# Performance work log

Hardware: AMD Instinct MI355X
Metric: run time of the kernel (lower is better)

## Reference

```python
import jax, jax.numpy as jnp
import numpy as np

N = 256          # spatial_dim
NC = 3           # components: u, v, density
INNER = 10       # inner_steps
DX = 2.0 * np.pi / N
VISC = 1e-3


def _van_leer(r):
    # classic van Leer limiter: (r+|r|)/(1+|r|)
    return jnp.where(r > 0, 2.0 * r / (1.0 + r), 0.0)


def _advect(c, u, v, dt):
    """van-Leer flux-limited advection tendency -div(vel*c) on a periodic grid.
    TVD blend of upwind (low-order) and Lax-Wendroff (high-order) face fluxes."""
    tend = jnp.zeros_like(c)
    for ax, vel in ((-2, u), (-1, v)):
        uf = 0.5 * (vel + jnp.roll(vel, -1, ax))   # face velocity at i+1/2
        cn = jnp.roll(c, -1, ax)
        dc = cn - c
        f_low = jnp.where(uf >= 0, uf * c, uf * cn)                      # upwind
        f_high = uf * 0.5 * (c + cn) - 0.5 * uf * uf * (dt / DX) * dc    # Lax-Wendroff
        dc_up = jnp.where(uf >= 0, c - jnp.roll(c, 1, ax), jnp.roll(c, -2, ax) - cn)
        dc_safe = jnp.where(jnp.abs(dc) > 1e-12, dc, 1e-12)
        phi = _van_leer(dc_up / dc_safe)
        flux = f_low + phi * (f_high - f_low)
        tend = tend - (flux - jnp.roll(flux, 1, ax)) / DX
    return tend


def _laplacian(x):
    return (jnp.roll(x, 1, -1) + jnp.roll(x, -1, -1)
            + jnp.roll(x, 1, -2) + jnp.roll(x, -1, -2) - 4.0 * x) / (DX * DX)


def _inv_fd_laplacian_eigs():
    # eigenvalues of the periodic FD laplacian, pseudo-inverse (zero mean mode)
    k = np.arange(N)
    lam1 = (2.0 * np.cos(2.0 * np.pi * k / N) - 2.0) / (DX * DX)
    lam = lam1[:, None] + lam1[None, :]
    lam[0, 0] = 1.0
    inv = 1.0 / lam
    inv[0, 0] = 0.0
    return jnp.asarray(inv, dtype=jnp.float32)

_INV_LAM = _inv_fd_laplacian_eigs()


def _project(u, v):
    """Pressure projection: remove divergence via FFT Poisson solve (periodic)."""
    div = (u - jnp.roll(u, 1, -2)) / DX + (v - jnp.roll(v, 1, -1)) / DX  # backward diff
    q = jnp.real(jnp.fft.ifft2(jnp.fft.fft2(div) * _INV_LAM))
    gu = (jnp.roll(q, -1, -2) - q) / DX   # forward diff (adjoint of div)
    gv = (jnp.roll(q, -1, -1) - q) / DX
    return u - gu, v - gv


def _inner_step(state, dt):
    u, v, d = state
    # velocity: explicit van-Leer convection + explicit diffusion, then projection
    u1 = u + dt * (_advect(u, u, v, dt) + VISC * _laplacian(u))
    v1 = v + dt * (_advect(v, u, v, dt) + VISC * _laplacian(v))
    u1, v1 = _project(u1, v1)
    # density advected with the OLD velocity (matches module's inner_step_fn)
    d1 = d + dt * _advect(d, u, v, dt)
    return (u1, v1, d1)


def _repeated_step(state, dt):
    def body(s, _):
        return _inner_step(s, dt), None
    state, _ = jax.lax.scan(body, state, None, length=INNER)
    return state


def setup_inputs() -> dict:
    key = jax.random.key(0)
    y0 = 0.1 * jax.random.normal(key, (8, N * N * NC), dtype=jnp.float32)
    return {"y0": y0, "dt": jnp.float32(1e-3), "num_steps_forward": 8}


def reference(y0, dt, num_steps_forward):
    spatial = y0.reshape(-1, N, N, NC)           # [B,H,W,3]
    state0 = (spatial[..., 0], spatial[..., 1], spatial[..., 2])

    def body(s, _):
        s2 = _repeated_step(s, dt)
        return s2, s2
    _, traj = jax.lax.scan(body, state0, None, length=num_steps_forward)
    yt = jnp.stack(traj, axis=-1)                # [T,B,H,W,3]
    yt = jnp.swapaxes(yt, 0, 1)                  # [B,T,H,W,3]
    return yt.reshape(yt.shape[0], yt.shape[1], N * N * NC)
```

## Files before the change

### kernel.cpp

```cpp
#include <hip/hip_runtime.h>
#include <hip/hip_bf16.h>


#define NN 256
#define NM 255
#define FIELD (NN*NN)
#define BATCH 8
#define TOTAL (BATCH*FIELD)
#define ROWF2 264

constexpr float RDX  = 40.743665431525205f;
constexpr float VISC = 1e-3f;

__device__ __forceinline__ int rev8(int x) { return (int)(__brev((unsigned)x) >> 24); }
__device__ __forceinline__ int pdx(int x)  { return x + (x >> 5); }

__device__ __forceinline__ void wave_sync() {
  asm volatile("" ::: "memory");
  __builtin_amdgcn_wave_barrier();
}

__device__ __forceinline__ float decode_dt(const unsigned* dtw) {
  unsigned w = dtw[0];
  float cf = __uint_as_float(w);
  float cb = __uint_as_float((w & 0xFFFFu) << 16);
  bool v32 = (cf > 1e-8f) && (cf < 1.0f);
  bool vbf = (cb > 1e-8f) && (cb < 1.0f);
  return v32 ? cf : (vbf ? cb : 1e-3f);
}

__device__ __forceinline__ float face_flux(float uf, float cm, float c0,
                                           float cp, float cpp, float hdtdx) {
  float dc = cp - c0;
  float f_low  = (uf >= 0.0f) ? uf*c0 : uf*cp;
  float f_high = uf*0.5f*(c0+cp) - hdtdx*uf*uf*dc;
  float dc_up  = (uf >= 0.0f) ? (c0 - cm) : (cpp - cp);
  float dc_safe = (fabsf(dc) > 1e-12f) ? dc : 1e-12f;
  float phi = (dc_up * dc_safe > 0.0f) ? (2.0f*dc_up/(dc_up + dc_safe)) : 0.0f;
  return f_low + phi*(f_high - f_low);
}

template<int NEED_VD>
__device__ __forceinline__ void advect_point(
    const float* __restrict__ Ub, const float* __restrict__ Vb,
    const float* __restrict__ Db,
    int i, int j, float hdtdx, float dt,
    float& u1, float& v1, float& d1)
{
  int im2 = ((i-2)&NM)*NN, im1 = ((i-1)&NM)*NN, i0r = i*NN,
      ip1 = ((i+1)&NM)*NN, ip2 = ((i+2)&NM)*NN;
  int jm2 = (j-2)&NM, jm1 = (j-1)&NM, jp1 = (j+1)&NM, jp2 = (j+2)&NM;

  float u_c  = Ub[i0r+j];
  float u_im2= Ub[im2+j], u_im1 = Ub[im1+j], u_ip1 = Ub[ip1+j], u_ip2 = Ub[ip2+j];
  float u_jm2= Ub[i0r+jm2], u_jm1 = Ub[i0r+jm1], u_jp1 = Ub[i0r+jp1], u_jp2 = Ub[i0r+jp2];
  float v_c  = Vb[i0r+j];
  float v_jm1= Vb[i0r+jm1], v_jp1 = Vb[i0r+jp1];

  float ufI0 = 0.5f*(u_c + u_ip1);
  float ufIm = 0.5f*(u_im1 + u_c);
  float vfJ0 = 0.5f*(v_c + v_jp1);
  float vfJm = 0.5f*(v_jm1 + v_c);

  float tu = -(( face_flux(ufI0, u_im1, u_c, u_ip1, u_ip2, hdtdx)
               - face_flux(ufIm, u_im2, u_im1, u_c, u_ip1, hdtdx))
             + ( face_flux(vfJ0, u_jm1, u_c, u_jp1, u_jp2, hdtdx)
               - face_flux(vfJm, u_jm2, u_jm1, u_c, u_jp1, hdtdx))) * RDX;
  float lapu = (u_im1 + u_ip1 + u_jm1 + u_jp1 - 4.0f*u_c) * (RDX*RDX);
  u1 = u_c + dt*(tu + VISC*lapu);

  if (NEED_VD) {
    float v_im2= Vb[im2+j], v_im1 = Vb[im1+j], v_ip1 = Vb[ip1+j], v_ip2 = Vb[ip2+j];
    float v_jm2= Vb[i0r+jm2], v_jp2 = Vb[i0r+jp2];
    float d_c  = Db[i0r+j];
    float d_im2= Db[im2+j], d_im1 = Db[im1+j], d_ip1 = Db[ip1+j], d_ip2 = Db[ip2+j];
    float d_jm2= Db[i0r+jm2], d_jm1 = Db[i0r+jm1], d_jp1 = Db[i0r+jp1], d_jp2 = Db[i0r+jp2];

    float tv = -(( face_flux(ufI0, v_im1, v_c, v_ip1, v_ip2, hdtdx)
                 - face_flux(ufIm, v_im2, v_im1, v_c, v_ip1, hdtdx))
               + ( face_flux(vfJ0, v_jm1, v_c, v_jp1, v_jp2, hdtdx)
                 - face_flux(vfJm, v_jm2, v_jm1, v_c, v_jp1, hdtdx))) * RDX;
    float lapv = (v_im1 + v_ip1 + v_jm1 + v_jp1 - 4.0f*v_c) * (RDX*RDX);
    v1 = v_c + dt*(tv + VISC*lapv);

    float td = -(( face_flux(ufI0, d_im1, d_c, d_ip1, d_ip2, hdtdx)
                 - face_flux(ufIm, d_im2, d_im1, d_c, d_ip1, hdtdx))
               + ( face_flux(vfJ0, d_jm1, d_c, d_jp1, d_jp2, hdtdx)
                 - face_flux(vfJm, d_jm2, d_jm1, d_c, d_jp1, hdtdx))) * RDX;
    d1 = d_c + dt*td;
  }
}

template<int NEED_VD>
__device__ __forceinline__ void advect_point_lds(
    const float* __restrict__ U, const float* __restrict__ V,
    const float* __restrict__ D,
    int ku, int kv, int j, float hdtdx, float dt,
    float& u1, float& v1, float& d1)
{
  int jm2 = (j-2)&NM, jm1 = (j-1)&NM, jp1 = (j+1)&NM, jp2 = (j+2)&NM;

  const float* Ur = U + ku*NN;
  float u_c  = Ur[j];
  float u_im2= U[(ku-2)*NN+j], u_im1 = U[(ku-1)*NN+j],
        u_ip1= U[(ku+1)*NN+j], u_ip2 = U[(ku+2)*NN+j];
  float u_jm2= Ur[jm2], u_jm1 = Ur[jm1], u_jp1 = Ur[jp1], u_jp2 = Ur[jp2];
  const float* Vr = V + kv*NN;
  float v_c  = Vr[j];
  float v_jm1= Vr[jm1], v_jp1 = Vr[jp1];

  float ufI0 = 0.5f*(u_c + u_ip1);
  float ufIm = 0.5f*(u_im1 + u_c);
  float vfJ0 = 0.5f*(v_c + v_jp1);
  float vfJm = 0.5f*(v_jm1 + v_c);

  float tu = -(( face_flux(ufI0, u_im1, u_c, u_ip1, u_ip2, hdtdx)
               - face_flux(ufIm, u_im2, u_im1, u_c, u_ip1, hdtdx))
             + ( face_flux(vfJ0, u_jm1, u_c, u_jp1, u_jp2, hdtdx)
               - face_flux(vfJm, u_jm2, u_jm1, u_c, u_jp1, hdtdx))) * RDX;
  float lapu = (u_im1 + u_ip1 + u_jm1 + u_jp1 - 4.0f*u_c) * (RDX*RDX);
  u1 = u_c + dt*(tu + VISC*lapu);

  if (NEED_VD) {
    float v_im2= V[(kv-2)*NN+j], v_im1 = V[(kv-1)*NN+j],
          v_ip1= V[(kv+1)*NN+j], v_ip2 = V[(kv+2)*NN+j];
    float v_jm2= Vr[jm2], v_jp2 = Vr[jp2];
    const float* Dr = D + kv*NN;
    float d_c  = Dr[j];
    float d_im2= D[(kv-2)*NN+j], d_im1 = D[(kv-1)*NN+j],
          d_ip1= D[(kv+1)*NN+j], d_ip2 = D[(kv+2)*NN+j];
    float d_jm2= Dr[jm2], d_jm1 = Dr[jm1], d_jp1 = Dr[jp1], d_jp2 = Dr[jp2];

    float tv = -(( face_flux(ufI0, v_im1, v_c, v_ip1, v_ip2, hdtdx)
                 - face_flux(ufIm, v_im2, v_im1, v_c, v_ip1, hdtdx))
               + ( face_flux(vfJ0, v_jm1, v_c, v_jp1, v_jp2, hdtdx)
                 - face_flux(vfJm, v_jm2, v_jm1, v_c, v_jp1, hdtdx))) * RDX;
    float lapv = (v_im1 + v_ip1 + v_jm1 + v_jp1 - 4.0f*v_c) * (RDX*RDX);
    v1 = v_c + dt*(tv + VISC*lapv);

    float td = -(( face_flux(ufI0, d_im1, d_c, d_ip1, d_ip2, hdtdx)
                 - face_flux(ufIm, d_im2, d_im1, d_c, d_ip1, hdtdx))
               + ( face_flux(vfJ0, d_jm1, d_c, d_jp1, d_jp2, hdtdx)
                 - face_flux(vfJm, d_jm2, d_jm1, d_c, d_jp1, hdtdx))) * RDX;
    d1 = d_c + dt*td;
  }
}


__device__ __forceinline__ void r16_fwd_low(float2* x, const float2* tw) {
  #pragma unroll
  for (int s = 1; s <= 4; ++s) {
    int h = 1 << (s-1);
    #pragma unroll
    for (int b = 0; b < 8; ++b) {
      int q = b & (h-1);
      int t = ((b >> (s-1)) << s) + q;
      float2 w = tw[q << (8-s)];
      float2 a = x[t], c = x[t+h];
      float wbx = w.x*c.x - w.y*c.y, wby = w.x*c.y + w.y*c.x;
      x[t]   = make_float2(a.x+wbx, a.y+wby);
      x[t+h] = make_float2(a.x-wbx, a.y-wby);
    }
  }
}
__device__ __forceinline__ void r16_fwd_high(float2* x, int r, const float2* tw) {
  #pragma unroll
  for (int s = 5; s <= 8; ++s) {
    int hp = 1 << (s-5);
    #pragma unroll
    for (int b = 0; b < 8; ++b) {
      int qp = b & (hp-1);
      int t = ((b >> (s-5)) << (s-4)) + qp;
      float2 w = tw[(r + (qp<<4)) << (8-s)];
      float2 a = x[t], c = x[t+hp];
      float wbx = w.x*c.x - w.y*c.y, wby = w.x*c.y + w.y*c.x;
      x[t]    = make_float2(a.x+wbx, a.y+wby);
      x[t+hp] = make_float2(a.x-wbx, a.y-wby);
    }
  }
}
__device__ __forceinline__ void r16_inv_high(float2* x, int r, const float2* tw) {
  #pragma unroll
  for (int s = 8; s >= 5; --s) {
    int hp = 1 << (s-5);
    #pragma unroll
    for (int b = 0; b < 8; ++b) {
      int qp = b & (hp-1);
      int t = ((b >> (s-5)) << (s-4)) + qp;
      float2 w = tw[(r + (qp<<4)) << (8-s)];
      float2 a = x[t], c = x[t+hp];
      float dx = a.x-c.x, dy = a.y-c.y;
      x[t]    = make_float2(a.x+c.x, a.y+c.y);
      x[t+hp] = make_float2(w.x*dx + w.y*dy, w.x*dy - w.y*dx);
    }
  }
}
__device__ __forceinline__ void r16_inv_low(float2* x, const float2* tw) {
  #pragma unroll
  for (int s = 4; s >= 1; --s) {
    int h = 1 << (s-1);
    #pragma unroll
    for (int b = 0; b < 8; ++b) {
      int q = b & (h-1);
      int t = ((b >> (s-1)) << s) + q;
      float2 w = tw[q << (8-s)];
      float2 a = x[t], c = x[t+h];
      float dx = a.x-c.x, dy = a.y-c.y;
      x[t]   = make_float2(a.x+c.x, a.y+c.y);
      x[t+h] = make_float2(w.x*dx + w.y*dy, w.x*dy - w.y*dx);
    }
  }
}

__device__ __forceinline__ void fft256_fwd_f2(float2* __restrict__ A, int lane,
                                              const float2* __restrict__ tw,
                                              bool active)
{
  #pragma unroll
  for (int s = 1; s <= 8; s += 2) {
    if (active) {
      int half = 1 << (s-1);
      int q2 = lane & (half - 1);
      int i0 = ((lane >> (s-1)) << (s+1)) + q2;
      float2 a0 = A[pdx(i0)];
      float2 a1 = A[pdx(i0 + half)];
      float2 a2 = A[pdx(i0 + 2*half)];
      float2 a3 = A[pdx(i0 + 3*half)];
      float2 w1 = tw[q2 << (8 - s)];
      float wbx = w1.x*a1.x - w1.y*a1.y, wby = w1.x*a1.y + w1.y*a1.x;
      float2 b0 = make_float2(a0.x + wbx, a0.y + wby);
      float2 b1 = make_float2(a0.x - wbx, a0.y - wby);
      wbx = w1.x*a3.x - w1.y*a3.y; wby = w1.x*a3.y + w1.y*a3.x;
      float2 b2 = make_float2(a2.x + wbx, a2.y + wby);
      float2 b3 = make_float2(a2.x - wbx, a2.y - wby);
      float2 w2 = tw[q2 << (7 - s)];
      float2 w3 = tw[(q2 + half) << (7 - s)];
      wbx = w2.x*b2.x - w2.y*b2.y; wby = w2.x*b2.y + w2.y*b2.x;
      A[pdx(i0)]            = make_float2(b0.x + wbx, b0.y + wby);
      A[pdx(i0 + 2*half)]   = make_float2(b0.x - wbx, b0.y - wby);
      wbx = w3.x*b3.x - w3.y*b3.y; wby = w3.x*b3.y + w3.y*b3.x;
      A[pdx(i0 + half)]     = make_float2(b1.x + wbx, b1.y + wby);
      A[pdx(i0 + 3*half)]   = make_float2(b1.x - wbx, b1.y - wby);
    }
    wave_sync();
  }
}

__device__ __forceinline__ void fft256_inv_f2(float2* __restrict__ A, int lane,
                                              const float2* __restrict__ tw,
                                              bool active)
{
  #pragma unroll
  for (int s = 8; s >= 2; s -= 2) {
    if (active) {
      int h = 1 << (s-2);
      int q2 = lane & (h - 1);
      int i0 = ((lane >> (s-2)) << s) + q2;
      float2 a0 = A[pdx(i0)];
      float2 a1 = A[pdx(i0 + h)];
      float2 a2 = A[pdx(i0 + 2*h)];
      float2 a3 = A[pdx(i0 + 3*h)];
      float2 w1 = tw[q2 << (8 - s)];
      float2 w2 = tw[(q2 + h) << (8 - s)];
      float dx = a0.x - a2.x, dy = a0.y - a2.y;
      float2 b0 = make_float2(a0.x + a2.x, a0.y + a2.y);
      float2 b2 = make_float2(w1.x*dx + w1.y*dy, w1.x*dy - w1.y*dx);
      dx = a1.x - a3.x; dy = a1.y - a3.y;
      float2 b1 = make_float2(a1.x + a3.x, a1.y + a3.y);
      float2 b3 = make_float2(w2.x*dx + w2.y*dy, w2.x*dy - w2.y*dx);
      float2 w3 = tw[q2 << (9 - s)];
      dx = b0.x - b1.x; dy = b0.y - b1.y;
      A[pdx(i0)]       = make_float2(b0.x + b1.x, b0.y + b1.y);
      A[pdx(i0 + h)]   = make_float2(w3.x*dx + w3.y*dy, w3.x*dy - w3.y*dx);
      dx = b2.x - b3.x; dy = b2.y - b3.y;
      A[pdx(i0 + 2*h)] = make_float2(b2.x + b3.x, b2.y + b3.y);
      A[pdx(i0 + 3*h)] = make_float2(w3.x*dx + w3.y*dy, w3.x*dy - w3.y*dx);
    }
    wave_sync();
  }
}

template<int W>
__device__ __forceinline__ void fft256_dit_fwd(float2* __restrict__ A, int lane,
                                               const float2* __restrict__ tw,
                                               bool active)
{
  #pragma unroll
  for (int s = 1; s <= 8; ++s) {
    int half = 1 << (s-1);
    if (active) {
      #pragma unroll
      for (int r = 0; r < 128/W; ++r) {
        int bfly = lane + r*W;
        int q = bfly & (half - 1);
        int g = (bfly >> (s-1)) << s;
        float2 w = tw[q << (8 - s)];
        float2 a = A[pdx(g + q)];
        float2 b = A[pdx(g + q + half)];
        float wbx = w.x*b.x - w.y*b.y;
        float wby = w.x*b.y + w.y*b.x;
        A[pdx(g + q)]        = make_float2(a.x + wbx, a.y + wby);
        A[pdx(g + q + half)] = make_float2(a.x - wbx, a.y - wby);
      }
    }
    wave_sync();
  }
}

template<int W>
__device__ __forceinline__ void fft256_dif_inv(float2* __restrict__ A, int lane,
                                               const float2* __restrict__ tw,
                                               bool active)
{
  #pragma unroll
  for (int s = 8; s >= 1; --s) {
    int half = 1 << (s-1);
    if (active) {
      #pragma unroll
      for (int r = 0; r < 128/W; ++r) {
        int bfly = lane + r*W;
        int q = bfly & (half - 1);
        int g = (bfly >> (s-1)) << s;
        float2 w = tw[q << (8 - s)];
        float2 a = A[pdx(g + q)];
        float2 b = A[pdx(g + q + half)];
        float dx = a.x - b.x, dy = a.y - b.y;
        A[pdx(g + q)]        = make_float2(a.x + b.x, a.y + b.y);
        A[pdx(g + q + half)] = make_float2(w.x*dx + w.y*dy, w.x*dy - w.y*dx);
      }
    }
    wave_sync();
  }
}

__global__ __launch_bounds__(1024) void proj_advect_fft8(
    const float2* __restrict__ Sprev, const float* __restrict__ inb,
    float* __restrict__ outb, float2* __restrict__ Snew,
    float* __restrict__ out, const unsigned* __restrict__ dtw,
    int T, int tm1, int first)
{
  __shared__ float2 tw[128];
  __shared__ float2 AbS[14*ROWF2];
  __shared__ float  qs [14*NN];
  __shared__ float  Ucs[13*NN];
  __shared__ float  Vcs[12*NN];
  float* Dss = (float*)(AbS + 8*ROWF2);
  float* Vs  = qs;

  const int tid  = threadIdx.x;
  const int j    = tid & 255;
  const int qtr  = tid >> 8;
  const int b    = blockIdx.x >> 5;
  const int row0 = (blockIdx.x & 31) << 3;

  if (tid < 128) {
    float sw, cw;
    __sincosf(-0.02454369260617026f * (float)tid, &sw, &cw);
    tw[tid] = make_float2(cw, sw);
  }

  const float dt = decode_dt(dtw);
  const float hdtdx = 0.5f*dt*RDX;

  const float* Ub = inb + b*FIELD;
  const float* Vb = inb + TOTAL + b*FIELD;
  const float* Db = inb + 2*TOTAL + b*FIELD;
  float* Uo  = outb + b*FIELD;
  float* Vo  = outb + TOTAL + b*FIELD;
  float* Do_ = outb + 2*TOTAL + b*FIELD;

  float u_reg[4], v_reg[3], d_reg[3];
  #pragma unroll
  for (int m = 0; m < 4; ++m) {
    int e = tid + (m << 10);
    if (e < 13*NN) {
      int k = e >> 8, jj = e & 255;
      u_reg[m] = Ub[((row0 - 3 + k) & NM)*NN + jj];
    }
  }
  #pragma unroll
  for (int m = 0; m < 3; ++m) {
    int e = tid + (m << 10);
    int k = e >> 8, jj = e & 255;
    int gr = ((row0 - 2 + k) & NM)*NN;
    v_reg[m] = Vb[gr + jj];
    d_reg[m] = Db[gr + jj];
  }

  if (!first) {
    const float2* Sb = Sprev + b*FIELD;
    #pragma unroll
    for (int m = 0; m < 4; ++m) {
      int e = tid + (m << 10);
      if (e < 14*NN) {
        int k = e >> 8, jj = e & 255;
        AbS[k*ROWF2 + pdx(jj)] = Sb[((row0 - 3 + k) & NM)*NN + jj];
      }
    }
    __syncthreads();

    {
      const int g16 = tid >> 4;
      const int r   = tid & 15;
      if (g16 < 14) {
        float2* Ar = AbS + g16*ROWF2;
        float2 x[16];
        #pragma unroll
        for (int k = 0; k < 16; ++k) x[k] = Ar[pdx(r + (k<<4))];
        r16_inv_high(x, r, tw);
        #pragma unroll
        for (int k = 0; k < 16; ++k) Ar[pdx(r + (k<<4))] = x[k];
      }
      wave_sync();
      if (g16 < 14) {
        float2* Ar = AbS + g16*ROWF2;
        float2 x[16];
        #pragma unroll
        for (int t = 0; t < 16; ++t) x[t] = Ar[pdx((r<<4) + t)];
        r16_inv_low(x, tw);
        #pragma unroll
        for (int t = 0; t < 16; ++t) Ar[pdx((r<<4) + t)] = x[t];
      }
    }
    __syncthreads();

    #pragma unroll
    for (int m = 0; m < 4; ++m) {
      int e = tid + (m << 10);
      if (e < 14*NN) {
        int k = e >> 8, jj = e & 255;
        qs[k*NN + jj] = AbS[k*ROWF2 + pdx(rev8(jj))].x;
      }
    }
    __syncthreads();
  } else {
    __syncthreads();
  }

  #pragma unroll
  for (int m = 0; m < 4; ++m) {
    int e = tid + (m << 10);
    if (e < 13*NN) {
      int k = e >> 8, jj = e & 255;
      Ucs[e] = first ? u_reg[m]
                     : (u_reg[m] - (qs[(k+1)*NN + jj] - qs[k*NN + jj])*RDX);
    }
  }
  #pragma unroll
  for (int m = 0; m < 3; ++m) {
    int e = tid + (m << 10);
    int k = e >> 8, jj = e & 255;
    Vcs[e] = first ? v_reg[m]
                   : (v_reg[m] - (qs[(k+1)*NN + ((jj+1)&NM)] - qs[(k+1)*NN + jj])*RDX);
    Dss[e] = d_reg[m];
  }
  __syncthreads();

  if (tm1 >= 0) {
    #pragma unroll
    for (int m = 0; m < 2; ++m) {
      int e = tid + (m << 10);
      int k = e >> 8, jj = e & 255;
      int pos = (row0 + k)*NN + jj;
      size_t o = ((size_t)(b*T + tm1)*FIELD + pos)*3u;
      out[o]   = Ucs[(k+3)*NN + jj];
      out[o+1] = Vcs[(k+2)*NN + jj];
      out[o+2] = Dss[(k+2)*NN + jj];
    }
  }

  const int kbeg = (qtr << 1) - 1;
  float u1r[3];
  #pragma unroll
  for (int kk = 0; kk < 3; ++kk) {
    int k = kbeg + kk;
    int ku = k + 3, kv = k + 2;
    float u1, v1, d1;
    if (kk == 0) {
      advect_point_lds<0>(Ucs, Vcs, Dss, ku, kv, j, hdtdx, dt, u1, v1, d1);
    } else {
      advect_point_lds<1>(Ucs, Vcs, Dss, ku, kv, j, hdtdx, dt, u1, v1, d1);
      int gi = (row0 + k)*NN + j;
      Uo[gi] = u1; Vo[gi] = v1; Do_[gi] = d1;
      Vs[k*NN + j] = v1;
    }
    u1r[kk] = u1;
  }
  __syncthreads();

  {
    int jm1 = (j - 1) & NM, rj = rev8(j);
    #pragma unroll
    for (int m = 0; m < 2; ++m) {
      int k = (qtr << 1) + m;
      float dv = (u1r[m+1] - u1r[m] + Vs[k*NN + j] - Vs[k*NN + jm1]) * RDX;
      AbS[k*ROWF2 + pdx(rj)] = make_float2(dv, 0.0f);
    }
  }
  __syncthreads();

  {
    const int g16 = tid >> 4;
    const int r   = tid & 15;
    if (g16 < 8) {
      float2* Ar = AbS + g16*ROWF2;
      float2 x[16];
      #pragma unroll
      for (int t = 0; t < 16; ++t) x[t] = Ar[pdx((r<<4) + t)];
      r16_fwd_low(x, tw);
      #pragma unroll
      for (int t = 0; t < 16; ++t) Ar[pdx((r<<4) + t)] = x[t];
    }
    wave_sync();
    if (g16 < 8) {
      float2* Ar = AbS + g16*ROWF2;
      float2 x[16];
      #pragma unroll
      for (int k = 0; k < 16; ++k) x[k] = Ar[pdx(r + (k<<4))];
      r16_fwd_high(x, r, tw);
      #pragma unroll
      for (int k = 0; k < 16; ++k) Ar[pdx(r + (k<<4))] = x[k];
    }
  }
  __syncthreads();

  float2* So = Snew + b*FIELD;
  #pragma unroll
  for (int m = 0; m < 2; ++m) {
    int e = tid + (m << 10);
    int row = e >> 8, jj = e & 255;
    So[(row0 + row)*NN + jj] = AbS[row*ROWF2 + pdx(jj)];
  }
}

__global__ __launch_bounds__(512) void fft_cols(float2* __restrict__ S)
{
  __shared__ float2 Ab[8*ROWF2];
  __shared__ float2 tw[128];
  __shared__ float  lam[NN];
  int tid = threadIdx.x;
  int b = blockIdx.x >> 5;
  int col0 = (blockIdx.x & 31) << 3;

  if (tid < 128) {
    float sw, cw;
    __sincosf(-0.02454369260617026f * (float)tid, &sw, &cw);
    tw[tid] = make_float2(cw, sw);
  }
  if (tid < 256) {
    float s1 = __sinf(0.01227184630308512983f * (float)tid);
    lam[tid] = -4.0f * s1 * s1 * (RDX*RDX);
  }

  float2* Sb = S + b*FIELD;
  #pragma unroll
  for (int k = 0; k < 4; ++k) {
    int idx = tid + (k << 9);
    int i = idx >> 3, c = idx & 7;
    Ab[c*ROWF2 + pdx(rev8(i))] = Sb[i*NN + col0 + c];
  }
  __syncthreads();

  int g = tid >> 6, lane = tid & 63;
  fft256_fwd_f2(Ab + g*ROWF2, lane, tw, true);

  float l2 = lam[col0 + g];
  #pragma unroll
  for (int r = 0; r < 4; ++r) {
    int k1 = lane + (r << 6);
    float den = lam[k1] + l2;
    float sc = ((k1 | (col0 + g)) == 0) ? 0.0f : (1.0f/den);
    sc *= (1.0f/65536.0f);
    float2 v = Ab[g*ROWF2 + pdx(k1)];
    Ab[g*ROWF2 + pdx(k1)] = make_float2(v.x*sc, v.y*sc);
  }
  wave_sync();

  fft256_inv_f2(Ab + g*ROWF2, lane, tw, true);
  __syncthreads();

  #pragma unroll
  for (int k = 0; k < 4; ++k) {
    int idx = tid + (k << 9);
    int i = idx >> 3, c = idx & 7;
    Sb[i*NN + col0 + c] = Ab[c*ROWF2 + pdx(rev8(i))];
  }
}

__global__ __launch_bounds__(512) void advect_div_fft(
    const float* __restrict__ inb, float* __restrict__ outb,
    float2* __restrict__ S, float* __restrict__ out,
    const unsigned* __restrict__ dtw, int T, int tm1)
{
  __shared__ float  Vs[8][NN];
  __shared__ float2 AbS[8*ROWF2];
  __shared__ float2 tw[128];
  const int tid = threadIdx.x;
  const int j   = tid & 255;
  const int h   = tid >> 8;
  const int b    = blockIdx.x >> 5;
  const int row0 = (blockIdx.x & 31) << 3;

  if (tid < 128) {
    float sw, cw;
    __sincosf(-0.02454369260617026f * (float)tid, &sw, &cw);
    tw[tid] = make_float2(cw, sw);
  }

  const float* Ub = inb + b*FIELD;
  const float* Vb = inb + TOTAL + b*FIELD;
  const float* Db = inb + 2*TOTAL + b*FIELD;
  float* Uo  = outb + b*FIELD;
  float* Vo  = outb + TOTAL + b*FIELD;
  float* Do_ = outb + 2*TOTAL + b*FIELD;

  const float dt = decode_dt(dtw);
  const float hdtdx = 0.5f*dt*RDX;

  if (tm1 >= 0) {
    #pragma unroll
    for (int k = 0; k < 4; ++k) {
      int pos = (row0 + h*4 + k)*NN + j;
      size_t o = ((size_t)(b*T + tm1)*FIELD + pos)*3u;
      out[o]   = Ub[pos];
      out[o+1] = Vb[pos];
      out[o+2] = Db[pos];
    }
  }

  const int kbeg = h ? 3 : -1;
  float u1r[5];
  #pragma unroll
  for (int kk = 0; kk < 5; ++kk) {
    int k = kbeg + kk;
    int r = (row0 + k) & NM;
    float u1, v1, d1;
    if (kk == 0) {
      advect_point<0>(Ub, Vb, Db, r, j, hdtdx, dt, u1, v1, d1);
    } else {
      advect_point<1>(Ub, Vb, Db, r, j, hdtdx, dt, u1, v1, d1);
      int gi = r*NN + j;
      Uo[gi] = u1; Vo[gi] = v1; Do_[gi] = d1;
      Vs[k][j] = v1;
    }
    u1r[kk] = u1;
  }
  __syncthreads();

  {
    int jm1 = (j - 1) & NM, rj = rev8(j);
    #pragma unroll
    for (int m = 0; m < 4; ++m) {
      int k = h*4 + m;
      float dv = (u1r[m+1] - u1r[m] + Vs[k][j] - Vs[k][jm1]) * RDX;
      AbS[k*ROWF2 + pdx(rj)] = make_float2(dv, 0.0f);
    }
  }
  __syncthreads();

  const int g = tid >> 6, lane = tid & 63;
  fft256_dit_fwd<64>(AbS + g*ROWF2, lane, tw, true);
  __syncthreads();

  float2* Sb = S + b*FIELD;
  #pragma unroll
  for (int k = 0; k < 4; ++k) {
    int row = h*4 + k;
    Sb[(row0 + row)*NN + j] = AbS[row*ROWF2 + pdx(j)];
  }
}

__global__ __launch_bounds__(512) void fft_cols_r9(float2* __restrict__ S)
{
  __shared__ float2 Ab[8*ROWF2];
  __shared__ float2 tw[128];
  __shared__ float  lam[NN];
  int tid = threadIdx.x;
  int b = blockIdx.x >> 5;
  int col0 = (blockIdx.x & 31) << 3;

  if (tid < 128) {
    float sw, cw;
    __sincosf(-0.02454369260617026f * (float)tid, &sw, &cw);
    tw[tid] = make_float2(cw, sw);
  }
  if (tid < 256) {
    float s1 = __sinf(0.01227184630308512983f * (float)tid);
    lam[tid] = -4.0f * s1 * s1 * (RDX*RDX);
  }

  float2* Sb = S + b*FIELD;
  #pragma unroll
  for (int k = 0; k < 4; ++k) {
    int idx = tid + (k << 9);
    int i = idx >> 3, c = idx & 7;
    Ab[c*ROWF2 + pdx(rev8(i))] = Sb[i*NN + col0 + c];
  }
  __syncthreads();

  int g = tid >> 6, lane = tid & 63;
  fft256_dit_fwd<64>(Ab + g*ROWF2, lane, tw, true);

  float l2 = lam[col0 + g];
  #pragma unroll
  for (int r = 0; r < 4; ++r) {
    int k1 = lane + (r << 6);
    float den = lam[k1] + l2;
    float sc = ((k1 | (col0 + g)) == 0) ? 0.0f : (1.0f/den);
    sc *= (1.0f/65536.0f);
    float2 v = Ab[g*ROWF2 + pdx(k1)];
    Ab[g*ROWF2 + pdx(k1)] = make_float2(v.x*sc, v.y*sc);
  }
  wave_sync();

  fft256_dif_inv<64>(Ab + g*ROWF2, lane, tw, true);
  __syncthreads();

  #pragma unroll
  for (int k = 0; k < 4; ++k) {
    int idx = tid + (k << 9);
    int i = idx >> 3, c = idx & 7;
    Sb[i*NN + col0 + c] = Ab[c*ROWF2 + pdx(rev8(i))];
  }
}

__global__ __launch_bounds__(512) void fft_inv_correct(
    const float2* __restrict__ S, float* __restrict__ outb)
{
  __shared__ float2 Ab[9*ROWF2];
  __shared__ float  qs[9*NN];
  __shared__ float2 tw[128];
  int tid = threadIdx.x;
  int b = blockIdx.x >> 5;
  int row0 = (blockIdx.x & 31) << 3;

  if (tid < 128) {
    float sw, cw;
    __sincosf(-0.02454369260617026f * (float)tid, &sw, &cw);
    tw[tid] = make_float2(cw, sw);
  }

  const float2* Sb = S + b*FIELD;
  #pragma unroll
  for (int m = 0; m < 5; ++m) {
    int e = tid + m*512;
    if (e < 9*NN) {
      int k = e >> 8, j = e & 255;
      Ab[k*ROWF2 + pdx(j)] = Sb[((row0 + k) & NM)*NN + j];
    }
  }
  __syncthreads();

  int g = tid >> 5, lane = tid & 31;
  bool active = (g < 9);
  fft256_dif_inv<32>(Ab + (active ? g : 8)*ROWF2, lane, tw, active);
  __syncthreads();

  #pragma unroll
  for (int m = 0; m < 5; ++m) {
    int e = tid + m*512;
    if (e < 9*NN) {
      int k = e >> 8, j = e & 255;
      qs[k*NN + j] = Ab[k*ROWF2 + pdx(rev8(j))].x;
    }
  }
  __syncthreads();

  float* Ug = outb + b*FIELD;
  float* Vg = outb + TOTAL + b*FIELD;
  #pragma unroll
  for (int m = 0; m < 4; ++m) {
    int e = tid + m*512;
    int k = e >> 8, j = e & 255;
    int gi = (row0 + k)*NN + j;
    float q0 = qs[k*NN + j];
    float q1 = qs[(k+1)*NN + j];
    float qj = qs[k*NN + ((j+1) & NM)];
    Ug[gi] -= (q1 - q0)*RDX;
    Vg[gi] -= (qj - q0)*RDX;
  }
}

__global__ __launch_bounds__(256) void write_out_k(
    const float* __restrict__ U, const float* __restrict__ V, const float* __restrict__ D,
    float* __restrict__ out, int t, int T)
{
  int idx = blockIdx.x*256 + threadIdx.x;
  int b = idx >> 16;
  int pos = idx & (FIELD-1);
  size_t o = ((size_t)(b*T + t)*FIELD + pos)*3u;
  out[o]   = U[idx];
  out[o+1] = V[idx];
  out[o+2] = D[idx];
}

__global__ __launch_bounds__(256) void init_state(
    const float* __restrict__ y0,
    float* __restrict__ U, float* __restrict__ V, float* __restrict__ D)
{
  int idx = blockIdx.x*256 + threadIdx.x;
  U[idx] = y0[idx*3];
  V[idx] = y0[idx*3+1];
  D[idx] = y0[idx*3+2];
}

__device__ __forceinline__ void fft_fwd_sc(float2* A, int lane) {
  #pragma unroll
  for (int s = 1; s <= 8; ++s) {
    int half = 1 << (s-1);
    float angscale = -6.28318530717958647692f / (float)(2*half);
    #pragma unroll
    for (int r = 0; r < 4; ++r) {
      int bfly = lane + (r << 5);
      int q = bfly & (half - 1);
      int g = (bfly >> (s-1)) << s;
      float sw, cw; __sincosf(angscale * (float)q, &sw, &cw);
      float2 a = A[g+q], b = A[g+q+half];
      float wbx = cw*b.x - sw*b.y, wby = cw*b.y + sw*b.x;
      A[g+q] = make_float2(a.x+wbx, a.y+wby);
      A[g+q+half] = make_float2(a.x-wbx, a.y-wby);
    }
    __syncthreads();
  }
}
__device__ __forceinline__ void fft_inv_sc(float2* A, int lane) {
  #pragma unroll
  for (int s = 8; s >= 1; --s) {
    int half = 1 << (s-1);
    float angscale = 6.28318530717958647692f / (float)(2*half);
    #pragma unroll
    for (int r = 0; r < 4; ++r) {
      int bfly = lane + (r << 5);
      int q = bfly & (half - 1);
      int g = (bfly >> (s-1)) << s;
      float sw, cw; __sincosf(angscale * (float)q, &sw, &cw);
      float2 a = A[g+q], b = A[g+q+half];
      float dx = a.x-b.x, dy = a.y-b.y;
      A[g+q] = make_float2(a.x+b.x, a.y+b.y);
      A[g+q+half] = make_float2(cw*dx - sw*dy, cw*dy + sw*dx);
    }
    __syncthreads();
  }
}

__global__ __launch_bounds__(256) void advect_kernel_fb(
    const float* __restrict__ U, const float* __restrict__ V, const float* __restrict__ D,
    float* __restrict__ Uo, float* __restrict__ Vo, float* __restrict__ Do_,
    const unsigned* __restrict__ dtw)
{
  int idx = blockIdx.x*256 + threadIdx.x;
  int j = idx & NM, i = (idx >> 8) & NM, base = (idx >> 16) * FIELD;
  float dt = decode_dt(dtw);
  float u1, v1, d1;
  advect_point<1>(U + base, V + base, D + base, i, j, 0.5f*dt*RDX, dt, u1, v1, d1);
  Uo[idx] = u1; Vo[idx] = v1; Do_[idx] = d1;
}

__global__ __launch_bounds__(256) void fft_rows_div_fb(
    const float* __restrict__ U2, const float* __restrict__ V2, float2* __restrict__ S)
{
  __shared__ float2 Ab[8*NN];
  int tid = threadIdx.x, b = blockIdx.x >> 5, row0 = (blockIdx.x & 31) << 3;
  const float* Ub = U2 + b*FIELD;
  const float* Vb = V2 + b*FIELD;
  int jm1 = (tid - 1) & NM, rj = rev8(tid);
  #pragma unroll
  for (int k = 0; k < 8; ++k) {
    int row = row0 + k, rm1 = (row - 1) & NM;
    float dv = (Ub[row*NN + tid] - Ub[rm1*NN + tid]
              + Vb[row*NN + tid] - Vb[row*NN + jm1]) * RDX;
    Ab[(k<<8) + rj] = make_float2(dv, 0.0f);
  }
  __syncthreads();
  int g = tid >> 5, lane = tid & 31;
  fft_fwd_sc(Ab + (g<<8), lane);
  float2* Sb = S + b*FIELD;
  #pragma unroll
  for (int k = 0; k < 8; ++k)
    Sb[(row0 + k)*NN + tid] = Ab[(k<<8) + tid];
}

__global__ __launch_bounds__(256) void fft_cols_fb(float2* __restrict__ S)
{
  __shared__ float2 Ab[8*NN];
  int tid = threadIdx.x, b = blockIdx.x >> 5, col0 = (blockIdx.x & 31) << 3;
  float2* Sb = S + b*FIELD;
  #pragma unroll
  for (int k = 0; k < 8; ++k) {
    int idx = tid + (k << 8);
    int i = idx >> 3, c = idx & 7;
    Ab[(c<<8) + rev8(i)] = Sb[i*NN + col0 + c];
  }
  __syncthreads();
  int g = tid >> 5, lane = tid & 31;
  fft_fwd_sc(Ab + (g<<8), lane);
  int k2 = col0 + g;
  float s2 = __sinf(0.01227184630308512983f * (float)k2);
  float l2 = -4.0f * s2 * s2 * (RDX*RDX);
  #pragma unroll
  for (int r = 0; r < 8; ++r) {
    int k1 = lane + (r << 5);
    float s1 = __sinf(0.01227184630308512983f * (float)k1);
    float l1 = -4.0f * s1 * s1 * (RDX*RDX);
    float den = l1 + l2;
    float sc = ((k1 | k2) == 0) ? 0.0f : (1.0f/den);
    sc *= (1.0f/65536.0f);
    float2 v = Ab[(g<<8) + k1];
    Ab[(g<<8) + k1] = make_float2(v.x*sc, v.y*sc);
  }
  __syncthreads();
  fft_inv_sc(Ab + (g<<8), lane);
  #pragma unroll
  for (int k = 0; k < 8; ++k) {
    int idx = tid + (k << 8);
    int i = idx >> 3, c = idx & 7;
    Sb[i*NN + col0 + c] = Ab[(c<<8) + rev8(i)];
  }
}

__global__ __launch_bounds__(256) void fft_rows_inv_fb(
    const float2* __restrict__ S, float* __restrict__ Q)
{
  __shared__ float2 Ab[8*NN];
  int tid = threadIdx.x, b = blockIdx.x >> 5, row0 = (blockIdx.x & 31) << 3;
  const float2* Sb = S + b*FIELD;
  #pragma unroll
  for (int k = 0; k < 8; ++k)
    Ab[(k<<8) + tid] = Sb[(row0 + k)*NN + tid];
  __syncthreads();
  int g = tid >> 5, lane = tid & 31;
  fft_inv_sc(Ab + (g<<8), lane);
  float* Qb = Q + b*FIELD;
  int rj = rev8(tid);
  #pragma unroll
  for (int k = 0; k < 8; ++k)
    Qb[(row0 + k)*NN + tid] = Ab[(k<<8) + rj].x;
}

__global__ __launch_bounds__(256) void correct_uv_fb(
    float* __restrict__ U2, float* __restrict__ V2, const float* __restrict__ Q)
{
  int idx = blockIdx.x*256 + threadIdx.x;
  int j = idx & NM, i = (idx >> 8) & NM, base = (idx >> 16) * FIELD;
  const float* Qb = Q + base;
  float q0 = Qb[i*NN + j];
  float qi = Qb[((i+1)&NM)*NN + j];
  float qj = Qb[i*NN + ((j+1)&NM)];
  U2[idx] -= (qi - q0)*RDX;
  V2[idx] -= (qj - q0)*RDX;
}

extern "C" void kernel_launch(void* const* d_in, const int* in_sizes, int n_in,
                              void* d_out, int out_size, void* d_ws, size_t ws_size,
                              hipStream_t stream) {
  (void)in_sizes; (void)n_in;
  const float*    y0  = (const float*)d_in[0];
  const unsigned* dtw = (const unsigned*)d_in[1];
  float* out = (float*)d_out;

  int T = out_size / (3*FIELD*BATCH);
  if (T < 1) T = 1;

  float* wsf = (float*)d_ws;

  if (ws_size >= (size_t)10*TOTAL*sizeof(float)) {
    float* stA = wsf;
    float* stB = wsf + 3*TOTAL;
    float2* Sa = (float2*)(wsf + 6*TOTAL);
    float2* Sc = (float2*)(wsf + 8*TOTAL);

    init_state<<<TOTAL/256, 256, 0, stream>>>(y0, stA, stA+TOTAL, stA+2*TOTAL);
    float* inb  = stA;
    float* outb = stB;
    float2* Sr = Sa;
    float2* Sw = Sc;
    int step = 0;
    for (int t = 0; t < T; ++t) {
      for (int s = 0; s < 10; ++s) {
        int tm1 = (s == 0) ? (t - 1) : -1;
        proj_advect_fft8<<<256, 1024, 0, stream>>>(Sr, inb, outb, Sw, out,
                                                   dtw, T, tm1, step == 0);
        fft_cols<<<256, 512, 0, stream>>>(Sw);
        float*  t1 = inb; inb = outb; outb = t1;
        float2* t2 = Sr;  Sr  = Sw;   Sw  = t2;
        ++step;
      }
    }
    fft_inv_correct<<<256, 512, 0, stream>>>(Sr, inb);
    write_out_k<<<TOTAL/256, 256, 0, stream>>>(inb, inb+TOTAL, inb+2*TOTAL,
                                               out, T-1, T);
    return;
  }

  if (ws_size >= (size_t)8*TOTAL*sizeof(float)) {
    float2* S = (float2*)(wsf + 6*TOTAL);
    init_state<<<TOTAL/256, 256, 0, stream>>>(y0, wsf, wsf+TOTAL, wsf+2*TOTAL);
    float* inb = wsf;
    float* outb = wsf + 3*TOTAL;
    for (int t = 0; t < T; ++t) {
      for (int s = 0; s < 10; ++s) {
        int tm1 = (s == 0) ? (t - 1) : -1;
        advect_div_fft <<<256, 512, 0, stream>>>(inb, outb, S, out, dtw, T, tm1);
        fft_cols_r9    <<<256, 512, 0, stream>>>(S);
        fft_inv_correct<<<256, 512, 0, stream>>>(S, outb);
        float* tmp = inb; inb = outb; outb = tmp;
      }
    }
    write_out_k<<<TOTAL/256, 256, 0, stream>>>(inb, inb+TOTAL, inb+2*TOTAL,
                                               out, T-1, T);
    return;
  }

  float* bank0 = wsf;
  float* bank1 = wsf + 3*TOTAL;
  init_state<<<TOTAL/256, 256, 0, stream>>>(y0, bank0, bank0+TOTAL, bank0+2*TOTAL);
  float* inb = bank0;
  float* outb = bank1;
  for (int t = 0; t < T; ++t) {
    for (int s = 0; s < 10; ++s) {
      float *Ui = inb,  *Vi = inb + TOTAL,  *Di = inb + 2*TOTAL;
      float *Uo = outb, *Vo = outb + TOTAL, *Do_ = outb + 2*TOTAL;
      float2* S = (float2*)(inb + TOTAL);
      float*  Q = inb;
      advect_kernel_fb<<<TOTAL/256, 256, 0, stream>>>(Ui, Vi, Di, Uo, Vo, Do_, dtw);
      fft_rows_div_fb <<<BATCH*32, 256, 0, stream>>>(Uo, Vo, S);
      fft_cols_fb     <<<BATCH*32, 256, 0, stream>>>(S);
      fft_rows_inv_fb <<<BATCH*32, 256, 0, stream>>>(S, Q);
      correct_uv_fb   <<<TOTAL/256, 256, 0, stream>>>(Uo, Vo, Q);
      float* tmp = inb; inb = outb; outb = tmp;
    }
    write_out_k<<<TOTAL/256, 256, 0, stream>>>(inb, inb+TOTAL, inb+2*TOTAL, out, t, T);
  }
}
```

Baseline: 2.000 ms.

## Pack pairs of real rows into one complex FFT for row transforms

The row-direction FFTs are real-input (divergence) and real-output (pressure). This packs two real rows into one complex row, then separates them with Hermitian symmetry after the forward transform and combines them before the inverse. That halves the number of row FFTs and the LDS traffic for them. The cost is extra unpacking arithmetic, and only half of the threads now do FFT work in these phases.

```diff
diff --git a/kernel.cpp b/kernel.cpp
--- a/kernel.cpp
+++ b/kernel.cpp
@@ -390,11 +390,13 @@
   if (!first) {
     const float2* Sb = Sprev + b*FIELD;
     #pragma unroll
-    for (int m = 0; m < 4; ++m) {
+    for (int m = 0; m < 2; ++m) {
       int e = tid + (m << 10);
-      if (e < 14*NN) {
-        int k = e >> 8, jj = e & 255;
-        AbS[k*ROWF2 + pdx(jj)] = Sb[((row0 - 3 + k) & NM)*NN + jj];
+      if (e < 7*NN) {
+        int p = e >> 8, jj = e & 255;
+        float2 sa = Sb[((row0 - 3 + 2*p) & NM)*NN + jj];
+        float2 sc = Sb[((row0 - 2 + 2*p) & NM)*NN + jj];
+        AbS[p*ROWF2 + pdx(jj)] = make_float2(sa.x - sc.y, sa.y + sc.x);
       }
     }
     __syncthreads();
@@ -402,7 +404,7 @@
     {
       const int g16 = tid >> 4;
       const int r   = tid & 15;
-      if (g16 < 14) {
+      if (g16 < 7) {
         float2* Ar = AbS + g16*ROWF2;
         float2 x[16];
         #pragma unroll
@@ -412,7 +414,7 @@
         for (int k = 0; k < 16; ++k) Ar[pdx(r + (k<<4))] = x[k];
       }
       wave_sync();
-      if (g16 < 14) {
+      if (g16 < 7) {
         float2* Ar = AbS + g16*ROWF2;
         float2 x[16];
         #pragma unroll
@@ -425,11 +427,13 @@
     __syncthreads();
 
     #pragma unroll
-    for (int m = 0; m < 4; ++m) {
+    for (int m = 0; m < 2; ++m) {
       int e = tid + (m << 10);
-      if (e < 14*NN) {
-        int k = e >> 8, jj = e & 255;
-        qs[k*NN + jj] = AbS[k*ROWF2 + pdx(rev8(jj))].x;
+      if (e < 7*NN) {
+        int p = e >> 8, jj = e & 255;
+        float2 z = AbS[p*ROWF2 + pdx(rev8(jj))];
+        qs[(2*p)*NN + jj]   = z.x;
+        qs[(2*p+1)*NN + jj] = z.y;
       }
     }
     __syncthreads();
@@ -490,19 +494,18 @@
 
   {
     int jm1 = (j - 1) & NM, rj = rev8(j);
-    #pragma unroll
-    for (int m = 0; m < 2; ++m) {
-      int k = (qtr << 1) + m;
-      float dv = (u1r[m+1] - u1r[m] + Vs[k*NN + j] - Vs[k*NN + jm1]) * RDX;
-      AbS[k*ROWF2 + pdx(rj)] = make_float2(dv, 0.0f);
-    }
+    float dv0 = (u1r[1] - u1r[0]
+               + Vs[(2*qtr)*NN + j] - Vs[(2*qtr)*NN + jm1]) * RDX;
+    float dv1 = (u1r[2] - u1r[1]
+               + Vs[(2*qtr+1)*NN + j] - Vs[(2*qtr+1)*NN + jm1]) * RDX;
+    AbS[qtr*ROWF2 + pdx(rj)] = make_float2(dv0, dv1);
   }
   __syncthreads();
 
   {
     const int g16 = tid >> 4;
     const int r   = tid & 15;
-    if (g16 < 8) {
+    if (g16 < 4) {
       float2* Ar = AbS + g16*ROWF2;
       float2 x[16];
       #pragma unroll
@@ -512,7 +515,7 @@
       for (int t = 0; t < 16; ++t) Ar[pdx((r<<4) + t)] = x[t];
     }
     wave_sync();
-    if (g16 < 8) {
+    if (g16 < 4) {
       float2* Ar = AbS + g16*ROWF2;
       float2 x[16];
       #pragma unroll
@@ -529,7 +532,15 @@
   for (int m = 0; m < 2; ++m) {
     int e = tid + (m << 10);
     int row = e >> 8, jj = e & 255;
-    So[(row0 + row)*NN + jj] = AbS[row*ROWF2 + pdx(jj)];
+    int p = row >> 1;
+    float2 z  = AbS[p*ROWF2 + pdx(jj)];
+    float2 z2 = AbS[p*ROWF2 + pdx((256 - jj) & 255)];
+    float2 sv;
+    if ((row & 1) == 0)
+      sv = make_float2(0.5f*(z.x + z2.x), 0.5f*(z.y - z2.y));
+    else
+      sv = make_float2(0.5f*(z.y + z2.y), 0.5f*(z2.x - z.x));
+    So[(row0 + row)*NN + jj] = sv;
   }
 }
 
```

Measured after the change: 1.994 ms. About the same (-0.3%).
